# Optimization experiments

Hardware: AMD Instinct MI355X
Metric: run time of the kernel (lower is better)

## Reference

```python
import jax, jax.numpy as jnp
import numpy as np

N = 8192          # num nodes
E = 262144        # num edges
F_IN = 512        # dataset.num_features
HID = 256         # hidden_dim
C = 16            # dataset.num_classes
ALPHA = 1.0
GAMMA = 1.0
EPS = 0.4
LN_EPS = 1e-5


def setup_inputs() -> dict:
    key = jax.random.key(0)
    ks = jax.random.split(key, 16)
    x = jax.random.normal(ks[0], (N, F_IN), dtype=jnp.float32)
    edge_index = jax.random.randint(ks[1], (2, E), 0, N, dtype=jnp.int64)
    def lin(k, fan_in, fan_out):
        s = 1.0 / np.sqrt(fan_in)
        return jax.random.uniform(k, (fan_in, fan_out), jnp.float32, -s, s)
    return {
        "x": x,
        "edge_index": edge_index,
        "W0": lin(ks[2], F_IN, HID), "b0": jnp.zeros((HID,), jnp.float32),
        "ln0_g": jnp.ones((HID,), jnp.float32), "ln0_b": jnp.zeros((HID,), jnp.float32),
        "W1": lin(ks[3], HID, HID), "b1": jnp.zeros((HID,), jnp.float32),
        "ln1_g": jnp.ones((HID,), jnp.float32), "ln1_b": jnp.zeros((HID,), jnp.float32),
        "W2": lin(ks[4], HID, C), "b2": jnp.zeros((C,), jnp.float32),
    }


def _layernorm(h, g, b):
    mu = jnp.mean(h, axis=-1, keepdims=True)
    var = jnp.var(h, axis=-1, keepdims=True)
    return (h - mu) * jax.lax.rsqrt(var + LN_EPS) * g + b


def _hpf_weight_matrix(edge_index, n, dtype):
    # to_dense_adj with parallel-edge accumulation
    A = jnp.zeros((n, n), dtype).at[edge_index[0], edge_index[1]].add(jnp.asarray(1.0, dtype))
    eye = jnp.eye(n, dtype=dtype)
    A = GAMMA * A + ALPHA * eye
    # D^{-1/2} A D^{-1/2} as fused row/col scaling (same math as the two diag matmuls)
    dinv = jax.lax.rsqrt(jnp.sum(A, axis=1))
    A_hat = dinv[:, None] * A * dinv[None, :]
    # (eps - 1) I + (I - A_hat) == eps*I - A_hat ; keep only positive entries (edge extraction)
    U = EPS * eye - A_hat
    return jnp.where(U > 0, U, jnp.asarray(0.0, dtype))


def reference(x, edge_index, W0, b0, ln0_g, ln0_b, W1, b1, ln1_g, ln1_b, W2, b2):
    Wmat = _hpf_weight_matrix(edge_index, x.shape[0], x.dtype)
    # GCNConv(normalize=False): h' = scatter_{src->tgt}(w * (h@W)[src]) + bias == Wmat^T @ (h@W) + b
    def gcn(h, W, b):
        return Wmat.T @ (h @ W) + b
    h = gcn(x, W0, b0)
    h = _layernorm(jax.nn.relu(h), ln0_g, ln0_b)   # dropout p=0.0 -> identity
    h = gcn(h, W1, b1)
    h = _layernorm(jax.nn.relu(h), ln1_g, ln1_b)
    embedding = gcn(h, W2, b2)
    return embedding, jax.nn.log_softmax(embedding, axis=1)
```

## Files before the change

### kernel.cpp

```cpp
#include <hip/hip_runtime.h>

#define NN 8192
#define NE 262144
#define FIN 512
#define HIDN 256
#define NC 16
#define NHB 48

typedef __attribute__((ext_vector_type(8))) short bf16x8;
typedef __attribute__((ext_vector_type(4))) short bf16x4;
typedef __attribute__((ext_vector_type(4))) float f32x4;

static __device__ __forceinline__ unsigned short f2bf(float f) {
    union { float f; unsigned u; } v; v.f = f;
    unsigned r = v.u + 0x7FFFu + ((v.u >> 16) & 1u);
    return (unsigned short)(r >> 16);
}

template<int K, int N>
static __device__ __forceinline__ void pack_w(const float* __restrict__ W,
                                              unsigned short* __restrict__ Wp, int f) {
    constexpr int KC = K / 32;
    int lane = f & 63;
    int g = f >> 6;
    int kc = g % KC;
    int nt = g / KC;
    int n = nt * 16 + (lane & 15);
    int kbase = kc * 32 + (lane >> 4) * 8;
    bf16x8 v;
#pragma unroll
    for (int j = 0; j < 8; ++j) v[j] = (short)f2bf(W[(kbase + j) * N + n]);
    *(bf16x8*)&Wp[f * 8] = v;
}

__global__ __launch_bounds__(512) void work_kernel(
    const int* __restrict__ ei,
    const float* __restrict__ W0, const float* __restrict__ W1, const float* __restrict__ W2,
    int* __restrict__ cnt, int* __restrict__ partial,
    unsigned short* __restrict__ Wp0, unsigned short* __restrict__ Wp1,
    unsigned short* __restrict__ Wp2)
{
    __shared__ int hist[NN];
    const int tid = threadIdx.x, bid = blockIdx.x;
    if (bid < NHB) {
#pragma unroll
        for (int i = 0; i < NN / 512; ++i) hist[tid + i * 512] = 0;
        __syncthreads();
        const int4* s4 = (const int4*)ei;
        const int4* t4 = (const int4*)(ei + NE);
        const int p = bid * 512 + tid;
#pragma unroll
        for (int i = 0; i < 3; ++i) {
            int c = p + i * (NHB * 512);
            if (c < NE / 4) {
                int4 s = s4[c];
                int4 t = t4[c];
                atomicAdd(&hist[s.x], 1);
                atomicAdd(&hist[s.y], 1);
                atomicAdd(&hist[s.z], 1);
                atomicAdd(&hist[s.w], 1);
                if (s.x == t.x) atomicAdd(&cnt[NN + s.x], 1);
                if (s.y == t.y) atomicAdd(&cnt[NN + s.y], 1);
                if (s.z == t.z) atomicAdd(&cnt[NN + s.z], 1);
                if (s.w == t.w) atomicAdd(&cnt[NN + s.w], 1);
            }
        }
        __syncthreads();
#pragma unroll
        for (int i = 0; i < NN / 512; ++i)
            partial[bid * NN + tid + i * 512] = hist[tid + i * 512];
    } else {
        int gp = (bid - NHB) * 512 + tid;
        if (gp < 16384)       pack_w<512, 256>(W0, Wp0, gp);
        else if (gp < 24576)  pack_w<256, 256>(W1, Wp1, gp - 16384);
        else                  pack_w<256, 16 >(W2, Wp2, gp - 24576);
    }
}

static __device__ __forceinline__ void ln_epilogue(
    const f32x4 acc[2], const float* __restrict__ bias, const float* __restrict__ gam,
    const float* __restrict__ bet, const float wdr[4],
    int w, int quad, int l16,
    unsigned short* sH, float red[][16])
{
    float bv[2], gv[2], btv[2];
#pragma unroll
    for (int nt = 0; nt < 2; ++nt) {
        int col = w * 32 + nt * 16 + l16;
        bv[nt] = bias[col]; gv[nt] = gam[col]; btv[nt] = bet[col];
    }
    float vv[2][4], s[4], ss[4];
#pragma unroll
    for (int reg = 0; reg < 4; ++reg) {
        float ps = 0.f, pss = 0.f;
#pragma unroll
        for (int nt = 0; nt < 2; ++nt) {
            float v = fmaxf(fmaf(wdr[reg], acc[nt][reg], bv[nt]), 0.f);
            vv[nt][reg] = v;
            ps += v; pss += v * v;
        }
        s[reg] = ps; ss[reg] = pss;
    }
#pragma unroll
    for (int off = 1; off < 16; off <<= 1)
#pragma unroll
        for (int reg = 0; reg < 4; ++reg) {
            s[reg]  += __shfl_xor(s[reg],  off, 64);
            ss[reg] += __shfl_xor(ss[reg], off, 64);
        }
    if (l16 == 0) {
#pragma unroll
        for (int reg = 0; reg < 4; ++reg) {
            int rl = quad * 4 + reg;
            red[rl][w * 2]     = s[reg];
            red[rl][w * 2 + 1] = ss[reg];
        }
    }
    __syncthreads();
#pragma unroll
    for (int reg = 0; reg < 4; ++reg) {
        int rl = quad * 4 + reg;
        float ts = 0.f, tss = 0.f;
#pragma unroll
        for (int i = 0; i < 8; ++i) { ts += red[rl][2 * i]; tss += red[rl][2 * i + 1]; }
        float mu  = ts * (1.0f / 256.0f);
        float var = tss * (1.0f / 256.0f) - mu * mu;
        float rs  = rsqrtf(var + 1e-5f);
#pragma unroll
        for (int nt = 0; nt < 2; ++nt) {
            float o = (vv[nt][reg] - mu) * rs * gv[nt] + btv[nt];
            sH[rl * 264 + w * 32 + nt * 16 + l16] = f2bf(o);
        }
    }
    __syncthreads();
}

__global__ __launch_bounds__(512) void mega_kernel(
    const float* __restrict__ x,
    const unsigned short* __restrict__ Wp0, const unsigned short* __restrict__ Wp1,
    const unsigned short* __restrict__ Wp2,
    const float* __restrict__ b0, const float* __restrict__ g0, const float* __restrict__ be0,
    const float* __restrict__ b1, const float* __restrict__ g1, const float* __restrict__ be1,
    const float* __restrict__ b2, const int* __restrict__ cnt,
    const int* __restrict__ partial,
    float* __restrict__ out)
{
    __shared__ unsigned short sH[16 * 264];
    __shared__ float red[16][16];
    __shared__ float swd[16];

    const int tid  = threadIdx.x;
    const int lane = tid & 63, w = tid >> 6;
    const int quad = lane >> 4, l16 = lane & 15;
    const int row0 = blockIdx.x * 16;

    if (tid < 16) {
        int d = 0;
#pragma unroll
        for (int b = 0; b < NHB; ++b) d += partial[b * NN + row0 + tid];
        int base = cnt[2 * NN];
        int sl = cnt[NN + row0 + tid] - base;
        float u = 0.4f - (1.0f + (float)sl) / (1.0f + (float)d);
        swd[tid] = u > 0.0f ? u : 0.0f;
    }
    __syncthreads();
    float wdr[4];
#pragma unroll
    for (int reg = 0; reg < 4; ++reg) wdr[reg] = swd[quad * 4 + reg];

    const bf16x8* Wp0v = (const bf16x8*)Wp0;
    const bf16x8* Wp1v = (const bf16x8*)Wp1;
    const bf16x8* Wp2v = (const bf16x8*)Wp2;

    const float4* xr = (const float4*)x + (row0 + l16) * 128 + quad * 2;
    f32x4 acc[2];
#pragma unroll
    for (int nt = 0; nt < 2; ++nt) acc[nt] = (f32x4){0.f, 0.f, 0.f, 0.f};
#pragma unroll
    for (int kc = 0; kc < 16; ++kc) {
        float4 u0 = xr[kc * 8];
        float4 u1 = xr[kc * 8 + 1];
        bf16x8 a;
        a[0] = (short)f2bf(u0.x); a[1] = (short)f2bf(u0.y);
        a[2] = (short)f2bf(u0.z); a[3] = (short)f2bf(u0.w);
        a[4] = (short)f2bf(u1.x); a[5] = (short)f2bf(u1.y);
        a[6] = (short)f2bf(u1.z); a[7] = (short)f2bf(u1.w);
#pragma unroll
        for (int nt = 0; nt < 2; ++nt) {
            bf16x8 b = Wp0v[((w * 2 + nt) * 16 + kc) * 64 + lane];
            acc[nt] = __builtin_amdgcn_mfma_f32_16x16x32_bf16(a, b, acc[nt], 0, 0, 0);
        }
    }
    ln_epilogue(acc, b0, g0, be0, wdr, w, quad, l16, sH, red);

    f32x4 acc1[2];
#pragma unroll
    for (int nt = 0; nt < 2; ++nt) acc1[nt] = (f32x4){0.f, 0.f, 0.f, 0.f};
#pragma unroll
    for (int kc = 0; kc < 8; ++kc) {
        bf16x8 a = *(const bf16x8*)&sH[l16 * 264 + kc * 32 + quad * 8];
#pragma unroll
        for (int nt = 0; nt < 2; ++nt) {
            bf16x8 b = Wp1v[((w * 2 + nt) * 8 + kc) * 64 + lane];
            acc1[nt] = __builtin_amdgcn_mfma_f32_16x16x32_bf16(a, b, acc1[nt], 0, 0, 0);
        }
    }
    ln_epilogue(acc1, b1, g1, be1, wdr, w, quad, l16, sH, red);

    if (w == 0) {
        f32x4 acch = (f32x4){0.f, 0.f, 0.f, 0.f};
#pragma unroll
        for (int kc = 0; kc < 8; ++kc) {
            bf16x8 a = *(const bf16x8*)&sH[l16 * 264 + kc * 32 + quad * 8];
            bf16x8 b = Wp2v[kc * 64 + lane];
            acch = __builtin_amdgcn_mfma_f32_16x16x32_bf16(a, b, acch, 0, 0, 0);
        }
        float bb = b2[l16];
#pragma unroll
        for (int reg = 0; reg < 4; ++reg) {
            int row = row0 + quad * 4 + reg;
            float v = fmaf(wdr[reg], acch[reg], bb);
            float m = v;
#pragma unroll
            for (int off = 8; off >= 1; off >>= 1) m = fmaxf(m, __shfl_xor(m, off, 64));
            float e = __expf(v - m);
            float se = e;
#pragma unroll
            for (int off = 8; off >= 1; off >>= 1) se += __shfl_xor(se, off, 64);
            float lsm = (v - m) - __logf(se);
            out[row * 16 + l16] = v;
            out[NN * 16 + row * 16 + l16] = lsm;
        }
    }
}

extern "C" void kernel_launch(void* const* d_in, const int* in_sizes, int n_in,
                              void* d_out, int out_size, void* d_ws, size_t ws_size,
                              hipStream_t stream) {
    const float* x  = (const float*)d_in[0];
    const int*   ei = (const int*)d_in[1];
    const float* W0 = (const float*)d_in[2];
    const float* b0 = (const float*)d_in[3];
    const float* g0 = (const float*)d_in[4];
    const float* be0 = (const float*)d_in[5];
    const float* W1 = (const float*)d_in[6];
    const float* b1 = (const float*)d_in[7];
    const float* g1 = (const float*)d_in[8];
    const float* be1 = (const float*)d_in[9];
    const float* W2 = (const float*)d_in[10];
    const float* b2 = (const float*)d_in[11];
    float* out = (float*)d_out;

    char* ws = (char*)d_ws;
    int*            cnt = (int*)ws;
    unsigned short* Wp0 = (unsigned short*)(ws + 68 * 1024);
    unsigned short* Wp1 = (unsigned short*)(ws + 324 * 1024);
    unsigned short* Wp2 = (unsigned short*)(ws + 452 * 1024);
    int*        partial = (int*)(ws + 460 * 1024);

    work_kernel<<<NHB + 49, 512, 0, stream>>>(ei, W0, W1, W2, cnt, partial, Wp0, Wp1, Wp2);
    mega_kernel<<<NN / 16, 512, 0, stream>>>(x, Wp0, Wp1, Wp2,
                                             b0, g0, be0, b1, g1, be1, b2, cnt, partial, out);
}
```

Measured before the change: 110.4 us.

## Process 32 rows per block to reuse weight fragments across two M tiles

Each block now handles 32 node rows instead of 16, so every weight fragment loaded from global memory feeds two MFMAs, halving weight traffic per row. The x tile is loaded with coalesced float4 reads, converted to bf16 and staged in shared memory instead of being read strided per lane. The cost is twice the accumulator registers and more LDS, and the grid drops to 256 blocks, which may under-fill the GPU's compute units.

```diff
diff --git a/kernel.cpp b/kernel.cpp
--- a/kernel.cpp
+++ b/kernel.cpp
@@ -78,8 +78,8 @@
 }
 
 static __device__ __forceinline__ void ln_epilogue(
-    const f32x4 acc[2], const float* __restrict__ bias, const float* __restrict__ gam,
-    const float* __restrict__ bet, const float wdr[4],
+    const f32x4 acc[2][2], const float* __restrict__ bias, const float* __restrict__ gam,
+    const float* __restrict__ bet, const float wdr[2][4],
     int w, int quad, int l16,
     unsigned short* sH, float red[][16])
 {
@@ -89,49 +89,57 @@
         int col = w * 32 + nt * 16 + l16;
         bv[nt] = bias[col]; gv[nt] = gam[col]; btv[nt] = bet[col];
     }
-    float vv[2][4], s[4], ss[4];
-#pragma unroll
-    for (int reg = 0; reg < 4; ++reg) {
-        float ps = 0.f, pss = 0.f;
-#pragma unroll
-        for (int nt = 0; nt < 2; ++nt) {
-            float v = fmaxf(fmaf(wdr[reg], acc[nt][reg], bv[nt]), 0.f);
-            vv[nt][reg] = v;
-            ps += v; pss += v * v;
-        }
-        s[reg] = ps; ss[reg] = pss;
-    }
+    float vv[2][2][4], s[2][4], ss[2][4];
+#pragma unroll
+    for (int mt = 0; mt < 2; ++mt)
+#pragma unroll
+        for (int reg = 0; reg < 4; ++reg) {
+            float ps = 0.f, pss = 0.f;
+#pragma unroll
+            for (int nt = 0; nt < 2; ++nt) {
+                float v = fmaxf(fmaf(wdr[mt][reg], acc[mt][nt][reg], bv[nt]), 0.f);
+                vv[mt][nt][reg] = v;
+                ps += v; pss += v * v;
+            }
+            s[mt][reg] = ps; ss[mt][reg] = pss;
+        }
 #pragma unroll
     for (int off = 1; off < 16; off <<= 1)
 #pragma unroll
+        for (int mt = 0; mt < 2; ++mt)
+#pragma unroll
+            for (int reg = 0; reg < 4; ++reg) {
+                s[mt][reg]  += __shfl_xor(s[mt][reg],  off, 64);
+                ss[mt][reg] += __shfl_xor(ss[mt][reg], off, 64);
+            }
+    if (l16 == 0) {
+#pragma unroll
+        for (int mt = 0; mt < 2; ++mt)
+#pragma unroll
+            for (int reg = 0; reg < 4; ++reg) {
+                int rl = mt * 16 + quad * 4 + reg;
+                red[rl][w * 2]     = s[mt][reg];
+                red[rl][w * 2 + 1] = ss[mt][reg];
+            }
+    }
+    __syncthreads();
+#pragma unroll
+    for (int mt = 0; mt < 2; ++mt)
+#pragma unroll
         for (int reg = 0; reg < 4; ++reg) {
-            s[reg]  += __shfl_xor(s[reg],  off, 64);
-            ss[reg] += __shfl_xor(ss[reg], off, 64);
-        }
-    if (l16 == 0) {
-#pragma unroll
-        for (int reg = 0; reg < 4; ++reg) {
-            int rl = quad * 4 + reg;
-            red[rl][w * 2]     = s[reg];
-            red[rl][w * 2 + 1] = ss[reg];
-        }
-    }
-    __syncthreads();
-#pragma unroll
-    for (int reg = 0; reg < 4; ++reg) {
-        int rl = quad * 4 + reg;
-        float ts = 0.f, tss = 0.f;
-#pragma unroll
-        for (int i = 0; i < 8; ++i) { ts += red[rl][2 * i]; tss += red[rl][2 * i + 1]; }
-        float mu  = ts * (1.0f / 256.0f);
-        float var = tss * (1.0f / 256.0f) - mu * mu;
-        float rs  = rsqrtf(var + 1e-5f);
-#pragma unroll
-        for (int nt = 0; nt < 2; ++nt) {
-            float o = (vv[nt][reg] - mu) * rs * gv[nt] + btv[nt];
-            sH[rl * 264 + w * 32 + nt * 16 + l16] = f2bf(o);
-        }
-    }
+            int rl = mt * 16 + quad * 4 + reg;
+            float ts = 0.f, tss = 0.f;
+#pragma unroll
+            for (int i = 0; i < 8; ++i) { ts += red[rl][2 * i]; tss += red[rl][2 * i + 1]; }
+            float mu  = ts * (1.0f / 256.0f);
+            float var = tss * (1.0f / 256.0f) - mu * mu;
+            float rs  = rsqrtf(var + 1e-5f);
+#pragma unroll
+            for (int nt = 0; nt < 2; ++nt) {
+                float o = (vv[mt][nt][reg] - mu) * rs * gv[nt] + btv[nt];
+                sH[rl * 264 + w * 32 + nt * 16 + l16] = f2bf(o);
+            }
+        }
     __syncthreads();
 }
 
@@ -145,16 +153,26 @@
     const int* __restrict__ partial,
     float* __restrict__ out)
 {
-    __shared__ unsigned short sH[16 * 264];
-    __shared__ float red[16][16];
-    __shared__ float swd[16];
+    __shared__ unsigned short sX[32 * 520];
+    __shared__ unsigned short sH[32 * 264];
+    __shared__ float red[32][16];
+    __shared__ float swd[32];
 
     const int tid  = threadIdx.x;
     const int lane = tid & 63, w = tid >> 6;
     const int quad = lane >> 4, l16 = lane & 15;
-    const int row0 = blockIdx.x * 16;
-
-    if (tid < 16) {
+    const int row0 = blockIdx.x * 32;
+
+    const float4* x4 = (const float4*)x;
+    float4 v[8];
+#pragma unroll
+    for (int i = 0; i < 4; ++i) {
+        int idx = i * 1024 + tid * 2;
+        v[2 * i]     = x4[row0 * 128 + idx];
+        v[2 * i + 1] = x4[row0 * 128 + idx + 1];
+    }
+
+    if (tid < 32) {
         int d = 0;
 #pragma unroll
         for (int b = 0; b < NHB; ++b) d += partial[b * NN + row0 + tid];
@@ -163,72 +181,88 @@
         float u = 0.4f - (1.0f + (float)sl) / (1.0f + (float)d);
         swd[tid] = u > 0.0f ? u : 0.0f;
     }
+
+#pragma unroll
+    for (int i = 0; i < 4; ++i) {
+        int idx = i * 1024 + tid * 2;
+        int r = idx >> 7, c4 = idx & 127;
+        bf16x8 h;
+        h[0] = (short)f2bf(v[2 * i].x);     h[1] = (short)f2bf(v[2 * i].y);
+        h[2] = (short)f2bf(v[2 * i].z);     h[3] = (short)f2bf(v[2 * i].w);
+        h[4] = (short)f2bf(v[2 * i + 1].x); h[5] = (short)f2bf(v[2 * i + 1].y);
+        h[6] = (short)f2bf(v[2 * i + 1].z); h[7] = (short)f2bf(v[2 * i + 1].w);
+        *(bf16x8*)&sX[r * 520 + c4 * 4] = h;
+    }
     __syncthreads();
-    float wdr[4];
-#pragma unroll
-    for (int reg = 0; reg < 4; ++reg) wdr[reg] = swd[quad * 4 + reg];
+
+    float wdr[2][4];
+#pragma unroll
+    for (int mt = 0; mt < 2; ++mt)
+#pragma unroll
+        for (int reg = 0; reg < 4; ++reg) wdr[mt][reg] = swd[mt * 16 + quad * 4 + reg];
 
     const bf16x8* Wp0v = (const bf16x8*)Wp0;
     const bf16x8* Wp1v = (const bf16x8*)Wp1;
     const bf16x8* Wp2v = (const bf16x8*)Wp2;
 
-    const float4* xr = (const float4*)x + (row0 + l16) * 128 + quad * 2;
-    f32x4 acc[2];
-#pragma unroll
-    for (int nt = 0; nt < 2; ++nt) acc[nt] = (f32x4){0.f, 0.f, 0.f, 0.f};
+    f32x4 acc[2][2];
+#pragma unroll
+    for (int mt = 0; mt < 2; ++mt)
+#pragma unroll
+        for (int nt = 0; nt < 2; ++nt) acc[mt][nt] = (f32x4){0.f, 0.f, 0.f, 0.f};
 #pragma unroll
     for (int kc = 0; kc < 16; ++kc) {
-        float4 u0 = xr[kc * 8];
-        float4 u1 = xr[kc * 8 + 1];
-        bf16x8 a;
-        a[0] = (short)f2bf(u0.x); a[1] = (short)f2bf(u0.y);
-        a[2] = (short)f2bf(u0.z); a[3] = (short)f2bf(u0.w);
-        a[4] = (short)f2bf(u1.x); a[5] = (short)f2bf(u1.y);
-        a[6] = (short)f2bf(u1.z); a[7] = (short)f2bf(u1.w);
+        bf16x8 a0 = *(const bf16x8*)&sX[l16 * 520        + kc * 32 + quad * 8];
+        bf16x8 a1 = *(const bf16x8*)&sX[(16 + l16) * 520 + kc * 32 + quad * 8];
 #pragma unroll
         for (int nt = 0; nt < 2; ++nt) {
             bf16x8 b = Wp0v[((w * 2 + nt) * 16 + kc) * 64 + lane];
-            acc[nt] = __builtin_amdgcn_mfma_f32_16x16x32_bf16(a, b, acc[nt], 0, 0, 0);
+            acc[0][nt] = __builtin_amdgcn_mfma_f32_16x16x32_bf16(a0, b, acc[0][nt], 0, 0, 0);
+            acc[1][nt] = __builtin_amdgcn_mfma_f32_16x16x32_bf16(a1, b, acc[1][nt], 0, 0, 0);
         }
     }
     ln_epilogue(acc, b0, g0, be0, wdr, w, quad, l16, sH, red);
 
-    f32x4 acc1[2];
-#pragma unroll
-    for (int nt = 0; nt < 2; ++nt) acc1[nt] = (f32x4){0.f, 0.f, 0.f, 0.f};
+    f32x4 acc1[2][2];
+#pragma unroll
+    for (int mt = 0; mt < 2; ++mt)
+#pragma unroll
+        for (int nt = 0; nt < 2; ++nt) acc1[mt][nt] = (f32x4){0.f, 0.f, 0.f, 0.f};
 #pragma unroll
     for (int kc = 0; kc < 8; ++kc) {
-        bf16x8 a = *(const bf16x8*)&sH[l16 * 264 + kc * 32 + quad * 8];
+        bf16x8 a0 = *(const bf16x8*)&sH[l16 * 264        + kc * 32 + quad * 8];
+        bf16x8 a1 = *(const bf16x8*)&sH[(16 + l16) * 264 + kc * 32 + quad * 8];
 #pragma unroll
         for (int nt = 0; nt < 2; ++nt) {
             bf16x8 b = Wp1v[((w * 2 + nt) * 8 + kc) * 64 + lane];
-            acc1[nt] = __builtin_amdgcn_mfma_f32_16x16x32_bf16(a, b, acc1[nt], 0, 0, 0);
+            acc1[0][nt] = __builtin_amdgcn_mfma_f32_16x16x32_bf16(a0, b, acc1[0][nt], 0, 0, 0);
+            acc1[1][nt] = __builtin_amdgcn_mfma_f32_16x16x32_bf16(a1, b, acc1[1][nt], 0, 0, 0);
         }
     }
     ln_epilogue(acc1, b1, g1, be1, wdr, w, quad, l16, sH, red);
 
-    if (w == 0) {
+    if (w < 2) {
         f32x4 acch = (f32x4){0.f, 0.f, 0.f, 0.f};
 #pragma unroll
         for (int kc = 0; kc < 8; ++kc) {
-            bf16x8 a = *(const bf16x8*)&sH[l16 * 264 + kc * 32 + quad * 8];
+            bf16x8 a = *(const bf16x8*)&sH[(w * 16 + l16) * 264 + kc * 32 + quad * 8];
             bf16x8 b = Wp2v[kc * 64 + lane];
             acch = __builtin_amdgcn_mfma_f32_16x16x32_bf16(a, b, acch, 0, 0, 0);
         }
         float bb = b2[l16];
 #pragma unroll
         for (int reg = 0; reg < 4; ++reg) {
-            int row = row0 + quad * 4 + reg;
-            float v = fmaf(wdr[reg], acch[reg], bb);
-            float m = v;
+            int row = row0 + w * 16 + quad * 4 + reg;
+            float v2 = fmaf(wdr[w][reg], acch[reg], bb);
+            float m = v2;
 #pragma unroll
             for (int off = 8; off >= 1; off >>= 1) m = fmaxf(m, __shfl_xor(m, off, 64));
-            float e = __expf(v - m);
+            float e = __expf(v2 - m);
             float se = e;
 #pragma unroll
             for (int off = 8; off >= 1; off >>= 1) se += __shfl_xor(se, off, 64);
-            float lsm = (v - m) - __logf(se);
-            out[row * 16 + l16] = v;
+            float lsm = (v2 - m) - __logf(se);
+            out[row * 16 + l16] = v2;
             out[NN * 16 + row * 16 + l16] = lsm;
         }
     }
@@ -259,6 +293,6 @@
     int*        partial = (int*)(ws + 460 * 1024);
 
     work_kernel<<<NHB + 49, 512, 0, stream>>>(ei, W0, W1, W2, cnt, partial, Wp0, Wp1, Wp2);
-    mega_kernel<<<NN / 16, 512, 0, stream>>>(x, Wp0, Wp1, Wp2,
+    mega_kernel<<<NN / 32, 512, 0, stream>>>(x, Wp0, Wp1, Wp2,
                                              b0, g0, be0, b1, g1, be1, b2, cnt, partial, out);
 }
```

Measured after the change: 101.4 us (median of 2 runs). -8.2%, faster.
